# Optimization experiments

Hardware: AMD Instinct MI355X
Metric: run time of the kernel (lower is better)

Reference implementation:

```python
import jax, jax.numpy as jnp
import numpy as np
import math

HEADS = 16
DIMS = 1024
SEQ_LEN = 2048
RANK_K = 128
BATCH = 8


def setup_inputs() -> dict:
    key = jax.random.key(0)
    ks = jax.random.split(key, 14)
    dh_std = 1.0 / math.sqrt(DIMS)
    proj_std = 1.0 / math.sqrt(RANK_K)
    inp = {
        "q": jax.random.normal(ks[0], (BATCH, SEQ_LEN, DIMS), jnp.float32),
        "k": jax.random.normal(ks[1], (BATCH, SEQ_LEN, DIMS), jnp.float32),
        "v": jax.random.normal(ks[2], (BATCH, SEQ_LEN, DIMS), jnp.float32),
        # nn.Linear weights [out, in], bias [out]
        "Wq": jax.random.uniform(ks[3], (DIMS, DIMS), jnp.float32, -dh_std, dh_std),
        "bq": jax.random.uniform(ks[4], (DIMS,), jnp.float32, -dh_std, dh_std),
        "Wk": jax.random.uniform(ks[5], (DIMS, DIMS), jnp.float32, -dh_std, dh_std),
        "bk": jax.random.uniform(ks[6], (DIMS,), jnp.float32, -dh_std, dh_std),
        "Wv": jax.random.uniform(ks[7], (DIMS, DIMS), jnp.float32, -dh_std, dh_std),
        "bv": jax.random.uniform(ks[8], (DIMS,), jnp.float32, -dh_std, dh_std),
        # Linformer low-rank projections [seq_length, k], uniform(-1/sqrt(k), 1/sqrt(k))
        "proj_k": jax.random.uniform(ks[9], (SEQ_LEN, RANK_K), jnp.float32, -proj_std, proj_std),
        "proj_v": jax.random.uniform(ks[10], (SEQ_LEN, RANK_K), jnp.float32, -proj_std, proj_std),
        "Wo": jax.random.uniform(ks[11], (DIMS, DIMS), jnp.float32, -dh_std, dh_std),
        "bo": jax.random.uniform(ks[12], (DIMS,), jnp.float32, -dh_std, dh_std),
    }
    return inp


def reference(q, k, v, Wq, bq, Wk, bk, Wv, bv, proj_k, proj_v, Wo, bo):
    B, N, D = q.shape
    H = HEADS
    dh = D // H
    Kr = proj_k.shape[1]

    kp = k @ Wk.T + bk                       # [B, N, D]
    # faithful to original: plain reshape (view), NOT a head-split transpose
    qp = (q @ Wq.T + bq).reshape(B, H, N, dh)  # [B, H, N, dh]
    vp = v @ Wv.T + bv                       # [B, N, D]

    pk = jnp.einsum('bnd,nk->bkd', kp, proj_k[:N])  # [B, Kr, D]
    pv = jnp.einsum('bnd,nk->bkd', vp, proj_v[:N])  # [B, Kr, D]
    pk = pk.reshape(B, Kr, H, dh).transpose(0, 2, 1, 3)  # [B, H, Kr, dh]
    pv = pv.reshape(B, Kr, H, dh).transpose(0, 2, 1, 3)  # [B, H, Kr, dh]

    # scores [B,H,N,Kr] -> transposed to [B,H,Kr,N]; softmax over N (seq) axis
    scores = jnp.einsum('bhnd,bhkd->bhkn', qp, pk) / math.sqrt(dh)
    attn = jax.nn.softmax(scores, axis=-1)   # [B, H, Kr, N]
    out = jnp.einsum('bhkn,bhkd->bhnd', attn, pv)  # [B, H, N, dh]
    out = out.transpose(0, 2, 1, 3).reshape(B, N, D)
    return out @ Wo.T + bo
```

## Files before the change

### kernel.cpp

```cpp
#include <hip/hip_runtime.h>

typedef unsigned short u16;
typedef unsigned int   u32;
typedef __attribute__((ext_vector_type(4))) float fx4;
typedef __attribute__((ext_vector_type(8))) __bf16 bf16x8;
typedef __attribute__((ext_vector_type(8))) unsigned short us8;
typedef __attribute__((ext_vector_type(2))) unsigned int u32x2;

__device__ __forceinline__ u16 f2bf(float x){
  u32 u = __builtin_bit_cast(u32, x);
  u += 0x7fffu + ((u >> 16) & 1u);
  return (u16)(u >> 16);
}
__device__ __forceinline__ float b2f(u16 h){
  u32 u = ((u32)h) << 16;
  return __builtin_bit_cast(float, u);
}
__device__ __forceinline__ void gld16(const void* g, void* l){
  __builtin_amdgcn_global_load_lds(
      (const __attribute__((address_space(1))) u32*)g,
      (__attribute__((address_space(3))) u32*)l, 16, 0, 0);
}
__device__ __forceinline__ void xcd_remap(u32& bx, u32& by, u32& bz){
  u32 nx = gridDim.x, ny = gridDim.y, nz = gridDim.z;
  u32 nwg = nx * ny * nz;
  u32 orig = (blockIdx.z * ny + blockIdx.y) * nx + blockIdx.x;
  u32 lid = (orig & 7u) * (nwg >> 3) + (orig >> 3);
  bx = lid % nx;
  u32 rem = lid / nx;
  by = rem % ny;
  bz = rem / ny;
}

__global__ __launch_bounds__(256) void k_f2bf(const float* __restrict__ in,
                                              u16* __restrict__ out, int n8){
  int i = blockIdx.x * 256 + threadIdx.x;
  const int stride = gridDim.x * 256;
  for (; i < n8; i += stride){
    const float4* p = (const float4*)in + (long)i * 2;
    float4 a = p[0], b = p[1];
    us8 o = { f2bf(a.x), f2bf(a.y), f2bf(a.z), f2bf(a.w),
              f2bf(b.x), f2bf(b.y), f2bf(b.z), f2bf(b.w) };
    *((us8*)out + i) = o;
  }
}

__global__ __launch_bounds__(256) void k_f2bfW(const float* __restrict__ w0,
                                               const float* __restrict__ w1,
                                               const float* __restrict__ w2,
                                               const float* __restrict__ w3,
                                               u16* __restrict__ out,
                                               float* __restrict__ zbuf){
  if (blockIdx.x == 0 && blockIdx.y == 0) zbuf[threadIdx.x] = 0.f;
  const float* src = blockIdx.y == 0 ? w0 : blockIdx.y == 1 ? w1 :
                     blockIdx.y == 2 ? w2 : w3;
  u16* dst = out + (long)blockIdx.y * 1048576;
  int i = blockIdx.x * 256 + threadIdx.x;
  const int stride = gridDim.x * 256;
  for (; i < 131072; i += stride){
    const float4* p = (const float4*)src + (long)i * 2;
    float4 a = p[0], b = p[1];
    us8 o = { f2bf(a.x), f2bf(a.y), f2bf(a.z), f2bf(a.w),
              f2bf(b.x), f2bf(b.y), f2bf(b.z), f2bf(b.w) };
    *((us8*)dst + i) = o;
  }
}

__global__ __launch_bounds__(256) void k_tconv(const float* __restrict__ in,
                                               u16* __restrict__ out,
                                               int R, int C, long sIn, long sOut,
                                               float* __restrict__ colsum){
  in  += (long)blockIdx.z * sIn;
  out += (long)blockIdx.z * sOut;
  const int c0 = blockIdx.x * 64, r0 = blockIdx.y * 64;
  __shared__ u16 tile[64][66];
  __shared__ float red[256];
  const int t = threadIdx.x;
  const int cc = t & 63, wq = t >> 6;
  float part = 0.f;
  #pragma unroll
  for (int i = 0; i < 16; ++i){
    int rr = i * 4 + wq;
    float v = in[(long)(r0 + rr) * C + c0 + cc];
    tile[rr][cc] = f2bf(v);
    part += v;
  }
  if (colsum){
    red[t] = part;
    __syncthreads();
    if (t < 64){
      float s = red[t] + red[t + 64] + red[t + 128] + red[t + 192];
      atomicAdd(&colsum[c0 + t], s);
    }
  }
  __syncthreads();
  const int oc0 = t >> 5, jb = (t & 31) * 2;
  #pragma unroll
  for (int i = 0; i < 8; ++i){
    int oc = oc0 + i * 8;
    u32 pk2 = (u32)tile[jb][oc] | ((u32)tile[jb + 1][oc] << 16);
    *(u32*)(out + (long)(c0 + oc) * R + r0 + jb) = pk2;
  }
}

template<int BM, int BN, int MODE, int EPI, typename OutT>
__global__ __launch_bounds__(256) void k_gemm(
    const u16* __restrict__ A, int lda, long sAz,
    const u16* __restrict__ B, int ldb, long sBz,
    OutT* __restrict__ C, int ldc, long sCz,
    int K, const float* __restrict__ bias, const float* __restrict__ srow, float scale)
{
  constexpr int BK = 64;
  constexpr int FM = BM / 32, FN = BN / 32;
  __shared__ u16 ldsA[BM * BK];
  __shared__ u16 ldsB[BN * BK];
  u32 bx, by, bz;
  xcd_remap(bx, by, bz);
  const long z = bz;
  if constexpr (MODE == 0){ A += z * sAz; B += z * sBz; C += z * sCz; }
  const int t = threadIdx.x;
  const int lane = t & 63;
  const int w = t >> 6, wm = w >> 1, wn = w & 1;
  const int r15 = lane & 15, g = lane >> 4;
  const int m0 = by * BM, n0 = bx * BN;
  fx4 acc[FM][FN] = {};
  constexpr int CA = BM * BK / (8 * 256);
  constexpr int CB = BN * BK / (8 * 256);
  for (int kt = 0; kt < K; kt += BK){
    #pragma unroll
    for (int i = 0; i < CA; ++i){
      int ch = i * 256 + t, row = ch >> 3, cc = ch & 7;
      gld16(A + (long)(m0 + row) * lda + kt + cc * 8, (char*)ldsA + ch * 16);
    }
    #pragma unroll
    for (int i = 0; i < CB; ++i){
      int ch = i * 256 + t, row = ch >> 3, cc = ch & 7;
      gld16(B + (long)(n0 + row) * ldb + kt + cc * 8, (char*)ldsB + ch * 16);
    }
    __syncthreads();
    #pragma unroll
    for (int ks = 0; ks < 2; ++ks){
      bf16x8 af[FM], bfv[FN];
      #pragma unroll
      for (int mf = 0; mf < FM; ++mf)
        af[mf] = *(const bf16x8*)&ldsA[(wm * (BM/2) + mf * 16 + r15) * BK + ks * 32 + g * 8];
      #pragma unroll
      for (int nf = 0; nf < FN; ++nf)
        bfv[nf] = *(const bf16x8*)&ldsB[(wn * (BN/2) + nf * 16 + r15) * BK + ks * 32 + g * 8];
      #pragma unroll
      for (int mf = 0; mf < FM; ++mf)
        #pragma unroll
        for (int nf = 0; nf < FN; ++nf)
          acc[mf][nf] = __builtin_amdgcn_mfma_f32_16x16x32_bf16(af[mf], bfv[nf], acc[mf][nf], 0, 0, 0);
    }
    __syncthreads();
  }
  #pragma unroll
  for (int mf = 0; mf < FM; ++mf){
    #pragma unroll
    for (int nf = 0; nf < FN; ++nf){
      const int row0 = m0 + wm * (BM/2) + mf * 16 + g * 4;
      const int col  = n0 + wn * (BN/2) + nf * 16 + r15;
      float vv[4];
      #pragma unroll
      for (int r = 0; r < 4; ++r){
        float v = acc[mf][nf][r];
        if constexpr (EPI == 1) v += bias[col];
        if constexpr (EPI == 2) v = (v + srow[row0 + r] * bias[col]) * scale;
        if constexpr (EPI == 3) v = v + srow[row0 + r] * bias[col];
        vv[r] = v;
      }
      if constexpr (EPI == 3){
        u32 lo = (u32)f2bf(vv[0]) | ((u32)f2bf(vv[1]) << 16);
        u32 hi = (u32)f2bf(vv[2]) | ((u32)f2bf(vv[3]) << 16);
        u32x2 pk2 = { lo, hi };
        *(u32x2*)((u16*)C + (long)col * 128 + row0) = pk2;
      } else {
        #pragma unroll
        for (int r = 0; r < 4; ++r){
          if constexpr (sizeof(OutT) == 2) C[(long)(row0 + r) * ldc + col] = (OutT)f2bf(vv[r]);
          else                             C[(long)(row0 + r) * ldc + col] = (OutT)vv[r];
        }
      }
    }
  }
}

template<int EPI, typename OutT>
__global__ __launch_bounds__(512, 1) void k_gemm256(
    const u16* __restrict__ A, int lda,
    const u16* __restrict__ B, int ldb,
    OutT* __restrict__ C, int ldc,
    int K, const float* __restrict__ bias)
{
  constexpr int BM = 256, BN = 128, BK = 64;
  __shared__ u16 ldsA[3][BM * BK];
  __shared__ u16 ldsB[3][BN * BK];
  u32 bx, by, bz;
  xcd_remap(bx, by, bz);
  const int m0 = by * BM, n0 = bx * BN;
  const int t = threadIdx.x;
  const int lane = t & 63, w = t >> 6;
  const int wm = w >> 1, wn = w & 1;
  const int r15 = lane & 15, g = lane >> 4;
  const int NT = K >> 6;

  auto stageA = [&](int kt, int buf){
    #pragma unroll
    for (int j = 0; j < 4; ++j){
      int ch = j * 512 + t, row = ch >> 3, cc = ch & 7;
      gld16(A + (long)(m0 + row) * lda + kt + ((cc ^ (row & 7)) * 8),
            (char*)ldsA[buf] + ch * 16);
    }
  };
  auto stageB = [&](int kt, int buf){
    #pragma unroll
    for (int j = 0; j < 2; ++j){
      int ch = j * 512 + t, row = ch >> 3, cc = ch & 7;
      gld16(B + (long)(n0 + row) * ldb + kt + ((cc ^ (row & 7)) * 8),
            (char*)ldsB[buf] + ch * 16);
    }
  };

  stageA(0, 0); stageB(0, 0);
  if (NT > 1){
    stageA(BK, 1); stageB(BK, 1);
    asm volatile("s_waitcnt vmcnt(6)" ::: "memory");
  } else {
    asm volatile("s_waitcnt vmcnt(0)" ::: "memory");
  }
  __builtin_amdgcn_s_barrier();
  asm volatile("" ::: "memory");

  fx4 acc[4][4] = {};
  for (int tt = 0; tt < NT; ++tt){
    const u16* bA = ldsA[tt % 3];
    const u16* bB = ldsB[tt % 3];
    const int sbuf = (tt + 2) % 3;
    const bool pf = (tt + 2 < NT);
    bf16x8 af[2][4], bf[2][2];
    #pragma unroll
    for (int ks = 0; ks < 2; ++ks)
      #pragma unroll
      for (int mf = 0; mf < 4; ++mf)
        af[ks][mf] = *(const bf16x8*)((const char*)bA +
            (wm * 64 + mf * 16 + r15) * 128 + (((ks * 4 + g) ^ (r15 & 7)) * 16));
    #pragma unroll
    for (int ks = 0; ks < 2; ++ks)
      #pragma unroll
      for (int nf = 0; nf < 2; ++nf)
        bf[ks][nf] = *(const bf16x8*)((const char*)bB +
            (wn * 64 + nf * 16 + r15) * 128 + (((ks * 4 + g) ^ (r15 & 7)) * 16));
    if (pf) stageA((tt + 2) * BK, sbuf);
    asm volatile("" ::: "memory");
    __builtin_amdgcn_s_barrier();
    asm volatile("" ::: "memory");
    __builtin_amdgcn_s_setprio(1);
    #pragma unroll
    for (int ks = 0; ks < 2; ++ks)
      #pragma unroll
      for (int mf = 0; mf < 4; ++mf)
        #pragma unroll
        for (int nf = 0; nf < 2; ++nf)
          acc[mf][nf] = __builtin_amdgcn_mfma_f32_16x16x32_bf16(af[ks][mf], bf[ks][nf], acc[mf][nf], 0, 0, 0);
    __builtin_amdgcn_s_setprio(0);
    asm volatile("" ::: "memory");
    __builtin_amdgcn_s_barrier();
    asm volatile("" ::: "memory");
    bf16x8 bf2[2][2];
    #pragma unroll
    for (int ks = 0; ks < 2; ++ks)
      #pragma unroll
      for (int nf = 0; nf < 2; ++nf)
        bf2[ks][nf] = *(const bf16x8*)((const char*)bB +
            (wn * 64 + (nf + 2) * 16 + r15) * 128 + (((ks * 4 + g) ^ (r15 & 7)) * 16));
    if (pf) stageB((tt + 2) * BK, sbuf);
    __builtin_amdgcn_s_setprio(1);
    #pragma unroll
    for (int ks = 0; ks < 2; ++ks)
      #pragma unroll
      for (int mf = 0; mf < 4; ++mf)
        #pragma unroll
        for (int nf = 0; nf < 2; ++nf)
          acc[mf][nf + 2] = __builtin_amdgcn_mfma_f32_16x16x32_bf16(af[ks][mf], bf2[ks][nf], acc[mf][nf + 2], 0, 0, 0);
    __builtin_amdgcn_s_setprio(0);
    if (pf)                { asm volatile("s_waitcnt vmcnt(6)" ::: "memory"); }
    else if (tt + 1 < NT)  { asm volatile("s_waitcnt vmcnt(0)" ::: "memory"); }
    asm volatile("" ::: "memory");
    __builtin_amdgcn_s_barrier();
    asm volatile("" ::: "memory");
  }

  #pragma unroll
  for (int mf = 0; mf < 4; ++mf)
    #pragma unroll
    for (int nf = 0; nf < 4; ++nf){
      const int row0 = m0 + wm * 64 + mf * 16 + g * 4;
      const int col  = n0 + wn * 64 + nf * 16 + r15;
      float bcol = 0.f;
      if constexpr (EPI == 1) bcol = bias[col];
      #pragma unroll
      for (int r = 0; r < 4; ++r){
        float vv = acc[mf][nf][r] + bcol;
        if constexpr (sizeof(OutT) == 2) C[(long)(row0 + r) * ldc + col] = (OutT)f2bf(vv);
        else                             C[(long)(row0 + r) * ldc + col] = (OutT)vv;
      }
    }
}

__global__ __launch_bounds__(256) void k_gemmTN(
    const u16* __restrict__ projT, const float* __restrict__ ksrc,
    const float* __restrict__ vsrc, u16* __restrict__ ck)
{
  u32 bx, by, bz; xcd_remap(bx, by, bz);
  const int p = bz >> 3, b = bz & 7;
  const u16* A = projT + p * 262144 + by * 64 * 2048;
  const float* S = (p ? vsrc : ksrc) + (long)b * 2097152;
  u16* C = ck + p * 1048576 + b * 131072 + by * 64 * 1024;
  const int d0 = bx * 64;
  __shared__ u16 ldsA[2][64 * 64];
  __shared__ u16 ldsB[2][64 * 72];
  const int t = threadIdx.x, lane = t & 63, w = t >> 6;
  const int wm = w >> 1, wn = w & 1;
  const int r15 = lane & 15, g = lane >> 4;
  const int c4 = t & 15, r4 = t >> 4;

  auto ldA = [&](int kt, int buf){
    #pragma unroll
    for (int i = 0; i < 2; ++i){
      int ch = i * 256 + t, row = ch >> 3, cc = ch & 7;
      gld16(A + (long)row * 2048 + kt + ((cc ^ (row & 7)) * 8),
            (char*)ldsA[buf] + ch * 16);
    }
  };
  auto ldS = [&](int kt, float4* f){
    #pragma unroll
    for (int i = 0; i < 4; ++i)
      f[i] = *(const float4*)(S + (long)(kt + r4 * 4 + i) * 1024 + d0 + c4 * 4);
  };
  auto wrB = [&](const float4* f, int buf){
    #pragma unroll
    for (int j = 0; j < 4; ++j){
      u32 lo = (u32)f2bf(((const float*)&f[0])[j]) | ((u32)f2bf(((const float*)&f[1])[j]) << 16);
      u32 hi = (u32)f2bf(((const float*)&f[2])[j]) | ((u32)f2bf(((const float*)&f[3])[j]) << 16);
      u32x2 pr = { lo, hi };
      *(u32x2*)&ldsB[buf][(c4 * 4 + j) * 72 + r4 * 4] = pr;
    }
  };

  { float4 f0[4];
    ldS(0, f0); ldA(0, 0);
    asm volatile("s_waitcnt vmcnt(0)" ::: "memory");
    wrB(f0, 0); }
  __syncthreads();

  fx4 acc[2][2] = {};
  for (int tt = 0; tt < 32; ++tt){
    const int buf = tt & 1;
    const bool pf = (tt + 1 < 32);
    float4 fn[4];
    if (pf){ ldS((tt + 1) * 64, fn); ldA((tt + 1) * 64, buf ^ 1); }
    asm volatile("" ::: "memory");
    #pragma unroll
    for (int ks = 0; ks < 2; ++ks){
      bf16x8 af[2], bfv[2];
      #pragma unroll
      for (int mf = 0; mf < 2; ++mf){
        int row = wm * 32 + mf * 16 + r15;
        af[mf] = *(const bf16x8*)((const char*)ldsA[buf] + row * 128 +
                                  (((ks * 4 + g) ^ (row & 7)) * 16));
      }
      #pragma unroll
      for (int nf = 0; nf < 2; ++nf)
        bfv[nf] = *(const bf16x8*)&ldsB[buf][(wn * 32 + nf * 16 + r15) * 72 + ks * 32 + g * 8];
      #pragma unroll
      for (int mf = 0; mf < 2; ++mf)
        #pragma unroll
        for (int nf = 0; nf < 2; ++nf)
          acc[mf][nf] = __builtin_amdgcn_mfma_f32_16x16x32_bf16(af[mf], bfv[nf], acc[mf][nf], 0, 0, 0);
    }
    if (pf){
      asm volatile("s_waitcnt vmcnt(0)" ::: "memory");
      wrB(fn, buf ^ 1);
    }
    __syncthreads();
  }
  #pragma unroll
  for (int mf = 0; mf < 2; ++mf)
    #pragma unroll
    for (int nf = 0; nf < 2; ++nf){
      const int row0 = wm * 32 + mf * 16 + g * 4;
      const int col  = d0 + wn * 32 + nf * 16 + r15;
      #pragma unroll
      for (int r = 0; r < 4; ++r)
        C[(long)(row0 + r) * 1024 + col] = f2bf(acc[mf][nf][r]);
    }
}

__global__ __launch_bounds__(512) void k_stats(const u16* __restrict__ pk,
                                               const u16* __restrict__ qp,
                                               float* __restrict__ invZ){
  const int z = blockIdx.x;
  const int b = z >> 4, h = z & 15;
  const u16* pkh = pk + b * 131072 + h * 64;
  const u16* qph = qp + (long)z * 131072;
  __shared__ u16 pkL[128 * 64];
  __shared__ float zred[8][128];
  const int t = threadIdx.x, lane = t & 63, w = t >> 6;
  const int r15 = lane & 15, g = lane >> 4;
  #pragma unroll
  for (int i = 0; i < 2; ++i){
    int ch = i * 512 + t, row = ch >> 3, cc = ch & 7;
    int csrc = cc ^ (row & 7);
    gld16(pkh + (long)row * 1024 + csrc * 8, (char*)pkL + ch * 16);
  }
  __syncthreads();
  float zacc[8][4] = {};
  for (int c = 0; c < 8; ++c){
    const int n0 = w * 256 + c * 32;
    fx4 acc[8][2] = {};
    #pragma unroll
    for (int ks = 0; ks < 2; ++ks){
      bf16x8 bq[2];
      #pragma unroll
      for (int nf = 0; nf < 2; ++nf)
        bq[nf] = *(const bf16x8*)(qph + (long)(n0 + nf * 16 + r15) * 64 + ks * 32 + g * 8);
      #pragma unroll
      for (int mf = 0; mf < 8; ++mf){
        int row = mf * 16 + r15;
        int x = (ks * 4 + g) ^ (row & 7);
        bf16x8 a = *(const bf16x8*)((const char*)pkL + row * 128 + x * 16);
        #pragma unroll
        for (int nf = 0; nf < 2; ++nf)
          acc[mf][nf] = __builtin_amdgcn_mfma_f32_16x16x32_bf16(a, bq[nf], acc[mf][nf], 0, 0, 0);
      }
    }
    #pragma unroll
    for (int mf = 0; mf < 8; ++mf)
      #pragma unroll
      for (int nf = 0; nf < 2; ++nf)
        #pragma unroll
        for (int r = 0; r < 4; ++r)
          zacc[mf][r] += __expf(acc[mf][nf][r]);
  }
  #pragma unroll
  for (int mf = 0; mf < 8; ++mf)
    #pragma unroll
    for (int r = 0; r < 4; ++r){
      float v = zacc[mf][r];
      v += __shfl_xor(v, 1); v += __shfl_xor(v, 2);
      v += __shfl_xor(v, 4); v += __shfl_xor(v, 8);
      zacc[mf][r] = v;
    }
  if (r15 == 0){
    #pragma unroll
    for (int mf = 0; mf < 8; ++mf)
      #pragma unroll
      for (int r = 0; r < 4; ++r)
        zred[w][mf * 16 + g * 4 + r] = zacc[mf][r];
  }
  __syncthreads();
  if (t < 128){
    float s = 0.f;
    #pragma unroll
    for (int w2 = 0; w2 < 8; ++w2) s += zred[w2][t];
    invZ[(long)z * 128 + t] = 1.0f / s;
  }
}

__global__ __launch_bounds__(256) void k_attn(const u16* __restrict__ pk,
                                              const u16* __restrict__ qp,
                                              const u16* __restrict__ pvT,
                                              const float* __restrict__ invZ,
                                              u16* __restrict__ outh){
  u32 bx, by, bz;
  xcd_remap(bx, by, bz);
  const int z = by, nb = bx;
  const int b = z >> 4, h = z & 15;
  const u16* pkh = pk  + b * 131072 + h * 64;
  const u16* qph = qp  + (long)z * 131072;
  const u16* pvh = pvT + b * 131072 + h * 8192;
  const float* zh = invZ + (long)z * 128;
  __shared__ u16 pkL[128 * 64];
  __shared__ u16 ptL[4][32 * 132];
  __shared__ float zL[128];
  const int t = threadIdx.x, lane = t & 63, w = t >> 6;
  const int r15 = lane & 15, g = lane >> 4;
  #pragma unroll
  for (int i = 0; i < 4; ++i){
    int ch = i * 256 + t, row = ch >> 3, cc = ch & 7;
    int csrc = cc ^ (row & 7);
    gld16(pkh + (long)row * 1024 + csrc * 8, (char*)pkL + ch * 16);
  }
  if (t < 128) zL[t] = zh[t];
  __syncthreads();
  const int n0 = nb * 128 + w * 32;
  fx4 acc[8][2] = {};
  #pragma unroll
  for (int ks = 0; ks < 2; ++ks){
    bf16x8 bq[2];
    #pragma unroll
    for (int nf = 0; nf < 2; ++nf)
      bq[nf] = *(const bf16x8*)(qph + (long)(n0 + nf * 16 + r15) * 64 + ks * 32 + g * 8);
    #pragma unroll
    for (int mf = 0; mf < 8; ++mf){
      int row = mf * 16 + r15;
      int x = (ks * 4 + g) ^ (row & 7);
      bf16x8 a = *(const bf16x8*)((const char*)pkL + row * 128 + x * 16);
      #pragma unroll
      for (int nf = 0; nf < 2; ++nf)
        acc[mf][nf] = __builtin_amdgcn_mfma_f32_16x16x32_bf16(a, bq[nf], acc[mf][nf], 0, 0, 0);
    }
  }
  u16* pt = ptL[w];
  #pragma unroll
  for (int mf = 0; mf < 8; ++mf){
    const int kb = mf * 16 + g * 4;
    const float z0 = zL[kb], z1 = zL[kb + 1], z2 = zL[kb + 2], z3 = zL[kb + 3];
    #pragma unroll
    for (int nf = 0; nf < 2; ++nf){
      const int nl = nf * 16 + r15;
      u32 lo = (u32)f2bf(__expf(acc[mf][nf][0]) * z0) |
               ((u32)f2bf(__expf(acc[mf][nf][1]) * z1) << 16);
      u32 hi = (u32)f2bf(__expf(acc[mf][nf][2]) * z2) |
               ((u32)f2bf(__expf(acc[mf][nf][3]) * z3) << 16);
      u32x2 pkd = { lo, hi };
      *(u32x2*)(pt + nl * 132 + kb) = pkd;
    }
  }
  fx4 o[2][4] = {};
  #pragma unroll
  for (int ks = 0; ks < 4; ++ks){
    bf16x8 bv[4];
    #pragma unroll
    for (int nf = 0; nf < 4; ++nf)
      bv[nf] = *(const bf16x8*)(pvh + (long)(nf * 16 + r15) * 128 + ks * 32 + g * 8);
    #pragma unroll
    for (int mf = 0; mf < 2; ++mf){
      bf16x8 pa = *(const bf16x8*)(pt + (mf * 16 + r15) * 132 + ks * 32 + g * 8);
      #pragma unroll
      for (int nf = 0; nf < 4; ++nf)
        o[mf][nf] = __builtin_amdgcn_mfma_f32_16x16x32_bf16(pa, bv[nf], o[mf][nf], 0, 0, 0);
    }
  }
  u16* og = outh + ((long)b * 2048 + n0) * 1024 + h * 64;
  #pragma unroll
  for (int mf = 0; mf < 2; ++mf)
    #pragma unroll
    for (int nf = 0; nf < 4; ++nf)
      #pragma unroll
      for (int r = 0; r < 4; ++r){
        int nl = mf * 16 + g * 4 + r;
        og[(long)nl * 1024 + nf * 16 + r15] = f2bf(o[mf][nf][r]);
      }
}

extern "C" void kernel_launch(void* const* d_in, const int* in_sizes, int n_in,
                              void* d_out, int out_size, void* d_ws, size_t ws_size,
                              hipStream_t stream)
{
  const float* q   = (const float*)d_in[0];
  const float* k   = (const float*)d_in[1];
  const float* v   = (const float*)d_in[2];
  const float* Wq  = (const float*)d_in[3];
  const float* bq  = (const float*)d_in[4];
  const float* Wk  = (const float*)d_in[5];
  const float* bk  = (const float*)d_in[6];
  const float* Wv  = (const float*)d_in[7];
  const float* bv  = (const float*)d_in[8];
  const float* pjk = (const float*)d_in[9];
  const float* pjv = (const float*)d_in[10];
  const float* Wo  = (const float*)d_in[11];
  const float* bo  = (const float*)d_in[12];

  if (ws_size < 152044544u) return;

  char* ws = (char*)d_ws;
  u16*  q_bf  = (u16*)(ws + 0);
  float* invZ = (float*)(ws + 33554432);
  u16*  W_bf  = (u16*)(ws + 100663296);
  u16*  projT = (u16*)(ws + 109051904);
  float* sk   = (float*)(ws + 110100480);
  float* sv   = (float*)(ws + 110100992);
  u16*  qp    = (u16*)(ws + 110101504);
  u16*  ck    = (u16*)(ws + 143655936);
  u16*  pk    = (u16*)(ws + 147850240);
  u16*  pvT   = (u16*)(ws + 149947392);
  u16*  outh  = (u16*)(ws + 0);
  u16*  Wq_bf = W_bf, *Wk_bf = W_bf + 1048576, *Wv_bf = W_bf + 2097152, *Wo_bf = W_bf + 3145728;

  k_f2bf<<<2048, 256, 0, stream>>>(q, q_bf, 2097152);
  k_f2bfW<<<dim3(128,4), 256, 0, stream>>>(Wq, Wk, Wv, Wo, W_bf, sk);
  k_tconv<<<dim3(2,32,1),  256, 0, stream>>>(pjk, projT,          2048, 128, 0, 0, sk);
  k_tconv<<<dim3(2,32,1),  256, 0, stream>>>(pjv, projT + 262144, 2048, 128, 0, 0, sv);

  k_gemm256<1,u16><<<dim3(8,64), 512, 0, stream>>>(
      q_bf,1024, Wq_bf,1024, qp,1024, 1024, bq);
  k_gemmTN<<<dim3(16,2,16), 256, 0, stream>>>(projT, k, v, ck);
  k_gemm<64,64,0,2,u16><<<dim3(16,2,8), 256, 0, stream>>>(
      ck,1024,131072, Wk_bf,1024,0, pk,1024,131072, 1024, bk, sk, 0.125f);
  k_gemm<64,64,0,3,u16><<<dim3(16,2,8), 256, 0, stream>>>(
      ck + 1048576,1024,131072, Wv_bf,1024,0, pvT,0,131072, 1024, bv, sv, 1.f);
  k_stats<<<128, 512, 0, stream>>>(pk, qp, invZ);
  k_attn<<<dim3(16,128), 256, 0, stream>>>(pk, qp, pvT, invZ, outh);
  k_gemm256<1,float><<<dim3(8,64), 512, 0, stream>>>(
      outh,1024, Wo_bf,1024, (float*)d_out,1024, 1024, bo);
}
```

Baseline: 240.3 us.

## Triple-buffer TN projection GEMM with two-stage prefetch and swizzled B tile

The k_gemmTN kernel moves from double to triple LDS buffering. It now prefetches two K-tiles ahead, using partial vmcnt waits and raw s_barrier instead of a full drain each iteration. The transposed fp32-to-bf16 B tile now uses an XOR swizzle on its LDS writes and reads, to cut bank conflicts. This costs more LDS and registers per block, which may lower occupancy, and the hand-counted vmcnt values have to match the number of loads in flight.

```diff
diff --git a/kernel.cpp b/kernel.cpp
--- a/kernel.cpp
+++ b/kernel.cpp
@@ -4,6 +4,7 @@
 typedef unsigned int   u32;
 typedef __attribute__((ext_vector_type(4))) float fx4;
 typedef __attribute__((ext_vector_type(8))) __bf16 bf16x8;
+typedef __attribute__((ext_vector_type(4))) __bf16 bf16x4;
 typedef __attribute__((ext_vector_type(8))) unsigned short us8;
 typedef __attribute__((ext_vector_type(2))) unsigned int u32x2;
 
@@ -316,10 +317,10 @@
   const int p = bz >> 3, b = bz & 7;
   const u16* A = projT + p * 262144 + by * 64 * 2048;
   const float* S = (p ? vsrc : ksrc) + (long)b * 2097152;
-  u16* C = ck + p * 1048576 + b * 131072 + by * 64 * 1024;
+  u16* C = ck + p * 1048576 + b * 131072 + by * 65536;
   const int d0 = bx * 64;
-  __shared__ u16 ldsA[2][64 * 64];
-  __shared__ u16 ldsB[2][64 * 72];
+  __shared__ u16 ldsA[3][64 * 64];
+  __shared__ u16 ldsB[3][64 * 72];
   const int t = threadIdx.x, lane = t & 63, w = t >> 6;
   const int wm = w >> 1, wn = w & 1;
   const int r15 = lane & 15, g = lane >> 4;
@@ -341,26 +342,16 @@
   auto wrB = [&](const float4* f, int buf){
     #pragma unroll
     for (int j = 0; j < 4; ++j){
+      const int d = c4 * 4 + j;
       u32 lo = (u32)f2bf(((const float*)&f[0])[j]) | ((u32)f2bf(((const float*)&f[1])[j]) << 16);
       u32 hi = (u32)f2bf(((const float*)&f[2])[j]) | ((u32)f2bf(((const float*)&f[3])[j]) << 16);
       u32x2 pr = { lo, hi };
-      *(u32x2*)&ldsB[buf][(c4 * 4 + j) * 72 + r4 * 4] = pr;
+      *(u32x2*)&ldsB[buf][d * 72 + ((r4 ^ (d & 15)) * 4)] = pr;
     }
   };
 
-  { float4 f0[4];
-    ldS(0, f0); ldA(0, 0);
-    asm volatile("s_waitcnt vmcnt(0)" ::: "memory");
-    wrB(f0, 0); }
-  __syncthreads();
-
   fx4 acc[2][2] = {};
-  for (int tt = 0; tt < 32; ++tt){
-    const int buf = tt & 1;
-    const bool pf = (tt + 1 < 32);
-    float4 fn[4];
-    if (pf){ ldS((tt + 1) * 64, fn); ldA((tt + 1) * 64, buf ^ 1); }
-    asm volatile("" ::: "memory");
+  auto compute = [&](int buf){
     #pragma unroll
     for (int ks = 0; ks < 2; ++ks){
       bf16x8 af[2], bfv[2];
@@ -371,20 +362,60 @@
                                   (((ks * 4 + g) ^ (row & 7)) * 16));
       }
       #pragma unroll
-      for (int nf = 0; nf < 2; ++nf)
-        bfv[nf] = *(const bf16x8*)&ldsB[buf][(wn * 32 + nf * 16 + r15) * 72 + ks * 32 + g * 8];
+      for (int nf = 0; nf < 2; ++nf){
+        const int d = wn * 32 + nf * 16 + r15, x = d & 15;
+        const int q0 = ks * 8 + g * 2;
+        bf16x4 lo = *(const bf16x4*)&ldsB[buf][d * 72 + ((q0 ^ x) * 4)];
+        bf16x4 hi = *(const bf16x4*)&ldsB[buf][d * 72 + (((q0 + 1) ^ x) * 4)];
+        bfv[nf] = __builtin_shufflevector(lo, hi, 0, 1, 2, 3, 4, 5, 6, 7);
+      }
       #pragma unroll
       for (int mf = 0; mf < 2; ++mf)
         #pragma unroll
         for (int nf = 0; nf < 2; ++nf)
           acc[mf][nf] = __builtin_amdgcn_mfma_f32_16x16x32_bf16(af[mf], bfv[nf], acc[mf][nf], 0, 0, 0);
     }
-    if (pf){
-      asm volatile("s_waitcnt vmcnt(0)" ::: "memory");
-      wrB(fn, buf ^ 1);
-    }
-    __syncthreads();
-  }
+  };
+
+  float4 fa[4], fb[4];
+  ldS(0, fa); ldA(0, 0);
+  ldS(64, fb); ldA(64, 1);
+  asm volatile("s_waitcnt vmcnt(6)" ::: "memory");
+  wrB(fa, 0);
+  asm volatile("s_waitcnt lgkmcnt(0)" ::: "memory");
+  __builtin_amdgcn_s_barrier();
+  asm volatile("" ::: "memory");
+
+  for (int tt = 0; tt < 32; tt += 2){
+    {
+      const bool pf = (tt + 2 < 32);
+      if (pf){ ldS((tt + 2) * 64, fa); ldA((tt + 2) * 64, (tt + 2) % 3); }
+      asm volatile("" ::: "memory");
+      compute(tt % 3);
+      if (pf) { asm volatile("s_waitcnt vmcnt(6)" ::: "memory"); }
+      else    { asm volatile("s_waitcnt vmcnt(0)" ::: "memory"); }
+      wrB(fb, (tt + 1) % 3);
+      asm volatile("s_waitcnt lgkmcnt(0)" ::: "memory");
+      __builtin_amdgcn_s_barrier();
+      asm volatile("" ::: "memory");
+    }
+    {
+      const bool pf = (tt + 3 < 32);
+      const bool hv = (tt + 2 < 32);
+      if (pf){ ldS((tt + 3) * 64, fb); ldA((tt + 3) * 64, (tt + 3) % 3); }
+      asm volatile("" ::: "memory");
+      compute((tt + 1) % 3);
+      if (hv){
+        if (pf) { asm volatile("s_waitcnt vmcnt(6)" ::: "memory"); }
+        else    { asm volatile("s_waitcnt vmcnt(0)" ::: "memory"); }
+        wrB(fa, (tt + 2) % 3);
+      }
+      asm volatile("s_waitcnt lgkmcnt(0)" ::: "memory");
+      __builtin_amdgcn_s_barrier();
+      asm volatile("" ::: "memory");
+    }
+  }
+
   #pragma unroll
   for (int mf = 0; mf < 2; ++mf)
     #pragma unroll
```

Result: no change. 239.0 us (-0.5%).

## Pre-transpose k/v to bf16 and use generic GEMM for low-rank projection

Applied to the files above, without the earlier changes.

Replaces the fused fp32-reading k_gemmTN (which converted and transposed k/v inside the GEMM) with a separate transpose-convert kernel that writes k and v as bf16 in [D,N] layout. The projection then runs on the generic LDS-direct GEMM with 128x64 tiles. It also merges the two proj transposes into one launch and the pk/pv GEMMs into one k_pkpv launch. This adds a full extra pass writing and rereading 64MB of bf16 k/v in exchange for simpler, better-fed MFMA loads and fewer launches.

```diff
diff --git a/kernel.cpp b/kernel.cpp
--- a/kernel.cpp
+++ b/kernel.cpp
@@ -66,12 +66,39 @@
   }
 }
 
-__global__ __launch_bounds__(256) void k_tconv(const float* __restrict__ in,
-                                               u16* __restrict__ out,
-                                               int R, int C, long sIn, long sOut,
-                                               float* __restrict__ colsum){
-  in  += (long)blockIdx.z * sIn;
-  out += (long)blockIdx.z * sOut;
+__global__ __launch_bounds__(256) void k_tconvKV(const float* __restrict__ ksrc,
+                                                 const float* __restrict__ vsrc,
+                                                 u16* __restrict__ kT){
+  const int z = blockIdx.z;
+  const float* in = (z >= 8 ? vsrc : ksrc) + (long)(z & 7) * 2097152;
+  u16* out = kT + (long)(z >> 3) * 16777216 + (long)(z & 7) * 2097152;
+  const int c0 = blockIdx.x * 64, r0 = blockIdx.y * 64;
+  __shared__ u16 tile[64][66];
+  const int t = threadIdx.x;
+  const int cc = t & 63, wq = t >> 6;
+  #pragma unroll
+  for (int i = 0; i < 16; ++i){
+    int rr = i * 4 + wq;
+    tile[rr][cc] = f2bf(in[(long)(r0 + rr) * 1024 + c0 + cc]);
+  }
+  __syncthreads();
+  const int oc0 = t >> 5, jb = (t & 31) * 2;
+  #pragma unroll
+  for (int i = 0; i < 8; ++i){
+    int oc = oc0 + i * 8;
+    u32 pk2 = (u32)tile[jb][oc] | ((u32)tile[jb + 1][oc] << 16);
+    *(u32*)(out + (long)(c0 + oc) * 2048 + r0 + jb) = pk2;
+  }
+}
+
+__global__ __launch_bounds__(256) void k_tconvP(const float* __restrict__ pjk,
+                                                const float* __restrict__ pjv,
+                                                u16* __restrict__ projT,
+                                                float* __restrict__ ssum){
+  const int z = blockIdx.z;
+  const float* in = z ? pjv : pjk;
+  u16* out = projT + z * 262144;
+  float* colsum = ssum + z * 128;
   const int c0 = blockIdx.x * 64, r0 = blockIdx.y * 64;
   __shared__ u16 tile[64][66];
   __shared__ float red[256];
@@ -81,17 +108,15 @@
   #pragma unroll
   for (int i = 0; i < 16; ++i){
     int rr = i * 4 + wq;
-    float v = in[(long)(r0 + rr) * C + c0 + cc];
+    float v = in[(long)(r0 + rr) * 128 + c0 + cc];
     tile[rr][cc] = f2bf(v);
     part += v;
   }
-  if (colsum){
-    red[t] = part;
-    __syncthreads();
-    if (t < 64){
-      float s = red[t] + red[t + 64] + red[t + 128] + red[t + 192];
-      atomicAdd(&colsum[c0 + t], s);
-    }
+  red[t] = part;
+  __syncthreads();
+  if (t < 64){
+    float s = red[t] + red[t + 64] + red[t + 128] + red[t + 192];
+    atomicAdd(&colsum[c0 + t], s);
   }
   __syncthreads();
   const int oc0 = t >> 5, jb = (t & 31) * 2;
@@ -99,7 +124,7 @@
   for (int i = 0; i < 8; ++i){
     int oc = oc0 + i * 8;
     u32 pk2 = (u32)tile[jb][oc] | ((u32)tile[jb + 1][oc] << 16);
-    *(u32*)(out + (long)(c0 + oc) * R + r0 + jb) = pk2;
+    *(u32*)(out + (long)(c0 + oc) * 2048 + r0 + jb) = pk2;
   }
 }
 
@@ -118,6 +143,9 @@
   xcd_remap(bx, by, bz);
   const long z = bz;
   if constexpr (MODE == 0){ A += z * sAz; B += z * sBz; C += z * sCz; }
+  if constexpr (MODE == 3){ long p = z >> 3, bb = z & 7;
+                            A += p * 262144; B += p * 16777216 + bb * 2097152;
+                            C += p * 1048576 + bb * 131072; }
   const int t = threadIdx.x;
   const int lane = t & 63;
   const int w = t >> 6, wm = w >> 1, wn = w & 1;
@@ -166,21 +194,88 @@
       for (int r = 0; r < 4; ++r){
         float v = acc[mf][nf][r];
         if constexpr (EPI == 1) v += bias[col];
-        if constexpr (EPI == 2) v = (v + srow[row0 + r] * bias[col]) * scale;
-        if constexpr (EPI == 3) v = v + srow[row0 + r] * bias[col];
         vv[r] = v;
       }
-      if constexpr (EPI == 3){
+      #pragma unroll
+      for (int r = 0; r < 4; ++r){
+        if constexpr (sizeof(OutT) == 2) C[(long)(row0 + r) * ldc + col] = (OutT)f2bf(vv[r]);
+        else                             C[(long)(row0 + r) * ldc + col] = (OutT)vv[r];
+      }
+    }
+  }
+}
+
+__global__ __launch_bounds__(256) void k_pkpv(
+    const u16* __restrict__ ck, const u16* __restrict__ Wk_bf,
+    const u16* __restrict__ Wv_bf, const float* __restrict__ bk,
+    const float* __restrict__ bv, const float* __restrict__ ssum,
+    u16* __restrict__ pk, u16* __restrict__ pvT)
+{
+  constexpr int BM = 64, BN = 64, BK = 64;
+  __shared__ u16 ldsA[BM * BK];
+  __shared__ u16 ldsB[BN * BK];
+  u32 bx, by, bz;
+  xcd_remap(bx, by, bz);
+  const int half = bz >> 3, b = bz & 7;
+  const u16* A = ck + half * 1048576 + b * 131072;
+  const u16* B = half ? Wv_bf : Wk_bf;
+  const float* bias = half ? bv : bk;
+  const float* srow = ssum + half * 128;
+  const float scale = half ? 1.f : 0.125f;
+  const int t = threadIdx.x;
+  const int lane = t & 63;
+  const int w = t >> 6, wm = w >> 1, wn = w & 1;
+  const int r15 = lane & 15, g = lane >> 4;
+  const int m0 = by * BM, n0 = bx * BN;
+  fx4 acc[2][2] = {};
+  for (int kt = 0; kt < 1024; kt += BK){
+    #pragma unroll
+    for (int i = 0; i < 2; ++i){
+      int ch = i * 256 + t, row = ch >> 3, cc = ch & 7;
+      gld16(A + (long)(m0 + row) * 1024 + kt + cc * 8, (char*)ldsA + ch * 16);
+    }
+    #pragma unroll
+    for (int i = 0; i < 2; ++i){
+      int ch = i * 256 + t, row = ch >> 3, cc = ch & 7;
+      gld16(B + (long)(n0 + row) * 1024 + kt + cc * 8, (char*)ldsB + ch * 16);
+    }
+    __syncthreads();
+    #pragma unroll
+    for (int ks = 0; ks < 2; ++ks){
+      bf16x8 af[2], bfv[2];
+      #pragma unroll
+      for (int mf = 0; mf < 2; ++mf)
+        af[mf] = *(const bf16x8*)&ldsA[(wm * 32 + mf * 16 + r15) * BK + ks * 32 + g * 8];
+      #pragma unroll
+      for (int nf = 0; nf < 2; ++nf)
+        bfv[nf] = *(const bf16x8*)&ldsB[(wn * 32 + nf * 16 + r15) * BK + ks * 32 + g * 8];
+      #pragma unroll
+      for (int mf = 0; mf < 2; ++mf)
+        #pragma unroll
+        for (int nf = 0; nf < 2; ++nf)
+          acc[mf][nf] = __builtin_amdgcn_mfma_f32_16x16x32_bf16(af[mf], bfv[nf], acc[mf][nf], 0, 0, 0);
+    }
+    __syncthreads();
+  }
+  #pragma unroll
+  for (int mf = 0; mf < 2; ++mf){
+    #pragma unroll
+    for (int nf = 0; nf < 2; ++nf){
+      const int row0 = m0 + wm * 32 + mf * 16 + g * 4;
+      const int col  = n0 + wn * 32 + nf * 16 + r15;
+      float vv[4];
+      #pragma unroll
+      for (int r = 0; r < 4; ++r)
+        vv[r] = (acc[mf][nf][r] + srow[row0 + r] * bias[col]) * scale;
+      if (!half){
+        #pragma unroll
+        for (int r = 0; r < 4; ++r)
+          pk[b * 131072 + (long)(row0 + r) * 1024 + col] = f2bf(vv[r]);
+      } else {
         u32 lo = (u32)f2bf(vv[0]) | ((u32)f2bf(vv[1]) << 16);
         u32 hi = (u32)f2bf(vv[2]) | ((u32)f2bf(vv[3]) << 16);
         u32x2 pk2 = { lo, hi };
-        *(u32x2*)((u16*)C + (long)col * 128 + row0) = pk2;
-      } else {
-        #pragma unroll
-        for (int r = 0; r < 4; ++r){
-          if constexpr (sizeof(OutT) == 2) C[(long)(row0 + r) * ldc + col] = (OutT)f2bf(vv[r]);
-          else                             C[(long)(row0 + r) * ldc + col] = (OutT)vv[r];
-        }
+        *(u32x2*)(pvT + b * 131072 + (long)col * 128 + row0) = pk2;
       }
     }
   }
@@ -308,95 +403,6 @@
     }
 }
 
-__global__ __launch_bounds__(256) void k_gemmTN(
-    const u16* __restrict__ projT, const float* __restrict__ ksrc,
-    const float* __restrict__ vsrc, u16* __restrict__ ck)
-{
-  u32 bx, by, bz; xcd_remap(bx, by, bz);
-  const int p = bz >> 3, b = bz & 7;
-  const u16* A = projT + p * 262144 + by * 64 * 2048;
-  const float* S = (p ? vsrc : ksrc) + (long)b * 2097152;
-  u16* C = ck + p * 1048576 + b * 131072 + by * 64 * 1024;
-  const int d0 = bx * 64;
-  __shared__ u16 ldsA[2][64 * 64];
-  __shared__ u16 ldsB[2][64 * 72];
-  const int t = threadIdx.x, lane = t & 63, w = t >> 6;
-  const int wm = w >> 1, wn = w & 1;
-  const int r15 = lane & 15, g = lane >> 4;
-  const int c4 = t & 15, r4 = t >> 4;
-
-  auto ldA = [&](int kt, int buf){
-    #pragma unroll
-    for (int i = 0; i < 2; ++i){
-      int ch = i * 256 + t, row = ch >> 3, cc = ch & 7;
-      gld16(A + (long)row * 2048 + kt + ((cc ^ (row & 7)) * 8),
-            (char*)ldsA[buf] + ch * 16);
-    }
-  };
-  auto ldS = [&](int kt, float4* f){
-    #pragma unroll
-    for (int i = 0; i < 4; ++i)
-      f[i] = *(const float4*)(S + (long)(kt + r4 * 4 + i) * 1024 + d0 + c4 * 4);
-  };
-  auto wrB = [&](const float4* f, int buf){
-    #pragma unroll
-    for (int j = 0; j < 4; ++j){
-      u32 lo = (u32)f2bf(((const float*)&f[0])[j]) | ((u32)f2bf(((const float*)&f[1])[j]) << 16);
-      u32 hi = (u32)f2bf(((const float*)&f[2])[j]) | ((u32)f2bf(((const float*)&f[3])[j]) << 16);
-      u32x2 pr = { lo, hi };
-      *(u32x2*)&ldsB[buf][(c4 * 4 + j) * 72 + r4 * 4] = pr;
-    }
-  };
-
-  { float4 f0[4];
-    ldS(0, f0); ldA(0, 0);
-    asm volatile("s_waitcnt vmcnt(0)" ::: "memory");
-    wrB(f0, 0); }
-  __syncthreads();
-
-  fx4 acc[2][2] = {};
-  for (int tt = 0; tt < 32; ++tt){
-    const int buf = tt & 1;
-    const bool pf = (tt + 1 < 32);
-    float4 fn[4];
-    if (pf){ ldS((tt + 1) * 64, fn); ldA((tt + 1) * 64, buf ^ 1); }
-    asm volatile("" ::: "memory");
-    #pragma unroll
-    for (int ks = 0; ks < 2; ++ks){
-      bf16x8 af[2], bfv[2];
-      #pragma unroll
-      for (int mf = 0; mf < 2; ++mf){
-        int row = wm * 32 + mf * 16 + r15;
-        af[mf] = *(const bf16x8*)((const char*)ldsA[buf] + row * 128 +
-                                  (((ks * 4 + g) ^ (row & 7)) * 16));
-      }
-      #pragma unroll
-      for (int nf = 0; nf < 2; ++nf)
-        bfv[nf] = *(const bf16x8*)&ldsB[buf][(wn * 32 + nf * 16 + r15) * 72 + ks * 32 + g * 8];
-      #pragma unroll
-      for (int mf = 0; mf < 2; ++mf)
-        #pragma unroll
-        for (int nf = 0; nf < 2; ++nf)
-          acc[mf][nf] = __builtin_amdgcn_mfma_f32_16x16x32_bf16(af[mf], bfv[nf], acc[mf][nf], 0, 0, 0);
-    }
-    if (pf){
-      asm volatile("s_waitcnt vmcnt(0)" ::: "memory");
-      wrB(fn, buf ^ 1);
-    }
-    __syncthreads();
-  }
-  #pragma unroll
-  for (int mf = 0; mf < 2; ++mf)
-    #pragma unroll
-    for (int nf = 0; nf < 2; ++nf){
-      const int row0 = wm * 32 + mf * 16 + g * 4;
-      const int col  = d0 + wn * 32 + nf * 16 + r15;
-      #pragma unroll
-      for (int r = 0; r < 4; ++r)
-        C[(long)(row0 + r) * 1024 + col] = f2bf(acc[mf][nf][r]);
-    }
-}
-
 __global__ __launch_bounds__(512) void k_stats(const u16* __restrict__ pk,
                                                const u16* __restrict__ qp,
                                                float* __restrict__ invZ){
@@ -577,30 +583,29 @@
 
   char* ws = (char*)d_ws;
   u16*  q_bf  = (u16*)(ws + 0);
-  float* invZ = (float*)(ws + 33554432);
+  u16*  kT    = (u16*)(ws + 33554432);
+  u16*  vT    = (u16*)(ws + 67108864);
   u16*  W_bf  = (u16*)(ws + 100663296);
   u16*  projT = (u16*)(ws + 109051904);
   float* sk   = (float*)(ws + 110100480);
-  float* sv   = (float*)(ws + 110100992);
   u16*  qp    = (u16*)(ws + 110101504);
   u16*  ck    = (u16*)(ws + 143655936);
   u16*  pk    = (u16*)(ws + 147850240);
   u16*  pvT   = (u16*)(ws + 149947392);
+  float* invZ = (float*)(ws + 33554432);
   u16*  outh  = (u16*)(ws + 0);
   u16*  Wq_bf = W_bf, *Wk_bf = W_bf + 1048576, *Wv_bf = W_bf + 2097152, *Wo_bf = W_bf + 3145728;
 
   k_f2bf<<<2048, 256, 0, stream>>>(q, q_bf, 2097152);
   k_f2bfW<<<dim3(128,4), 256, 0, stream>>>(Wq, Wk, Wv, Wo, W_bf, sk);
-  k_tconv<<<dim3(2,32,1),  256, 0, stream>>>(pjk, projT,          2048, 128, 0, 0, sk);
-  k_tconv<<<dim3(2,32,1),  256, 0, stream>>>(pjv, projT + 262144, 2048, 128, 0, 0, sv);
+  k_tconvP<<<dim3(2,32,2), 256, 0, stream>>>(pjk, pjv, projT, sk);
+  k_tconvKV<<<dim3(16,32,16), 256, 0, stream>>>(k, v, kT);
 
   k_gemm256<1,u16><<<dim3(8,64), 512, 0, stream>>>(
       q_bf,1024, Wq_bf,1024, qp,1024, 1024, bq);
-  k_gemmTN<<<dim3(16,2,16), 256, 0, stream>>>(projT, k, v, ck);
-  k_gemm<64,64,0,2,u16><<<dim3(16,2,8), 256, 0, stream>>>(
-      ck,1024,131072, Wk_bf,1024,0, pk,1024,131072, 1024, bk, sk, 0.125f);
-  k_gemm<64,64,0,3,u16><<<dim3(16,2,8), 256, 0, stream>>>(
-      ck + 1048576,1024,131072, Wv_bf,1024,0, pvT,0,131072, 1024, bv, sv, 1.f);
+  k_gemm<128,64,3,0,u16><<<dim3(16,1,16), 256, 0, stream>>>(
+      projT,2048,0, kT,2048,0, ck,1024,0, 2048, nullptr, nullptr, 1.f);
+  k_pkpv<<<dim3(16,2,16), 256, 0, stream>>>(ck, Wk_bf, Wv_bf, bk, bv, sk, pk, pvT);
   k_stats<<<128, 512, 0, stream>>>(pk, qp, invZ);
   k_attn<<<dim3(16,128), 256, 0, stream>>>(pk, qp, pvT, invZ, outh);
   k_gemm256<1,float><<<dim3(8,64), 512, 0, stream>>>(
```

Result: slower. 260.5 us (+8.4%).
